# Optimization experiments

Hardware: AMD Instinct MI355X
Metric: run time of the kernel (lower is better)

Reference implementation:

```python
import jax, jax.numpy as jnp
import numpy as np


def setup_inputs() -> dict:
    key = jax.random.key(0)
    k1, k2, k3, k4 = jax.random.split(key, 4)
    b, c, h, w = 32, 512, 64, 64
    r = 16
    return {
        "x": jax.random.normal(k1, (b, c, h, w), dtype=jnp.float32),
        "mu": jax.random.uniform(k2, (b, 2), dtype=jnp.float32),
        "log_sigma_se": jnp.zeros((), dtype=jnp.float32),
        "w_fc1": jax.random.normal(k3, (c // r, c), dtype=jnp.float32) * 0.05,
        "w_fc2": jax.random.normal(k4, (c, c // r), dtype=jnp.float32) * 0.05,
    }


def reference(x, mu, log_sigma_se, w_fc1, w_fc2):
    b, c, h, w = x.shape
    sigma = jnp.exp(log_sigma_se)
    # grids in [0,1]; grid_x varies along h, grid_y along w ('ij' indexing)
    gx = jnp.linspace(0.0, 1.0, h)[:, None]          # (h,1)
    gy = jnp.linspace(0.0, 1.0, w)[None, :]          # (1,w)
    mu_h = mu[:, 0][:, None, None]                   # (b,1,1)
    mu_w = mu[:, 1][:, None, None]
    dx = gx[None, :, :] - mu_h                       # (b,h,w) via broadcast
    dy = gy[None, :, :] - mu_w
    kernel = jnp.exp(-(dx * dx + dy * dy) / (2.0 * sigma))   # (b,h,w)
    kernel = kernel / jnp.sum(kernel, axis=(1, 2), keepdims=True)
    squeezed = jnp.einsum('bchw,bhw->bc', x, kernel)          # (b,c)
    hid = jax.nn.relu(squeezed @ w_fc1.T)                     # (b,c//r)
    weights = jax.nn.sigmoid(hid @ w_fc2.T)                   # (b,c)
    return x * weights[:, :, None, None]
```

## Files before the change

### kernel.cpp

```cpp
#include <hip/hip_runtime.h>
#include <math.h>

#define BB 32
#define CC 512
#define HH 64
#define WW 64
#define RR 16
#define CR (CC / RR)
#define BPG 16
#define NGROUPS (BB / BPG)

typedef float floatx4 __attribute__((ext_vector_type(4)));

__device__ __forceinline__ float wave_sum64(float v) {
    #pragma unroll
    for (int off = 32; off > 0; off >>= 1)
        v += __shfl_xor(v, off, 64);
    return v;
}

__global__ void k_squeeze(const float* __restrict__ x,
                          const float* __restrict__ mu,
                          const float* __restrict__ log_sigma,
                          float* __restrict__ sq, int b0) {
    __shared__ float s_kx[64];
    __shared__ float s_ky[64];
    int b = b0 + blockIdx.y;
    int tid = threadIdx.x;

    if (tid < 64) {
        float sigma = expf(log_sigma[0]);
        float inv2s = 1.0f / (2.0f * sigma);
        float g = (float)tid / 63.0f;
        float dh = g - mu[b * 2 + 0];
        float dw = g - mu[b * 2 + 1];
        float vx = expf(-dh * dh * inv2s);
        float vy = expf(-dw * dw * inv2s);
        float sx = wave_sum64(vx);
        float sy = wave_sum64(vy);
        s_kx[tid] = vx / sx;
        s_ky[tid] = vy / sy;
    }
    __syncthreads();

    int wv = tid >> 6;
    int lane = tid & 63;
    int c = blockIdx.x * 4 + wv;
    const floatx4* xp = (const floatx4*)(x + ((size_t)(b * CC + c)) * (HH * WW));
    int col = lane & 15;
    int hbase = lane >> 4;
    float a0 = 0.f, a1 = 0.f, a2 = 0.f, a3 = 0.f;
    #pragma unroll
    for (int it = 0; it < 16; ++it) {
        int h = hbase + it * 4;
        floatx4 v = xp[h * 16 + col];
        float kh = s_kx[h];
        a0 += v.x * kh; a1 += v.y * kh; a2 += v.z * kh; a3 += v.w * kh;
    }
    int w0 = col * 4;
    float partial = a0 * s_ky[w0] + a1 * s_ky[w0 + 1] + a2 * s_ky[w0 + 2] + a3 * s_ky[w0 + 3];
    float s = wave_sum64(partial);
    if (lane == 0) sq[b * CC + c] = s;
}

__global__ void k_scale_fused(const float* __restrict__ x,
                              const float* __restrict__ sq,
                              const float* __restrict__ w1,
                              const float* __restrict__ w2,
                              float* __restrict__ out, int b0) {
    __shared__ float s_sq[CC];
    __shared__ float s_hid[CR];
    __shared__ float s_w[8];
    int b = b0 + blockIdx.y;
    int c0 = blockIdx.x * 8;
    int tid = threadIdx.x;

    for (int i = tid; i < CC; i += 256) s_sq[i] = sq[b * CC + i];
    __syncthreads();

    {
        int j = tid >> 3;
        int seg = tid & 7;
        float acc = 0.f;
        const float* w1r = w1 + j * CC + seg * 64;
        const float* sqr = s_sq + seg * 64;
        #pragma unroll 8
        for (int c = 0; c < 64; ++c) acc += sqr[c] * w1r[c];
        acc += __shfl_xor(acc, 4, 64);
        acc += __shfl_xor(acc, 2, 64);
        acc += __shfl_xor(acc, 1, 64);
        if (seg == 0) s_hid[j] = fmaxf(acc, 0.0f);
    }
    __syncthreads();

    if (tid < 8) {
        const float* w2r = w2 + (c0 + tid) * CR;
        float a = 0.f;
        #pragma unroll
        for (int jj = 0; jj < CR; ++jj) a += s_hid[jj] * w2r[jj];
        s_w[tid] = 1.0f / (1.0f + expf(-a));
    }
    __syncthreads();

    const floatx4* xp = (const floatx4*)(x + ((size_t)(b * CC + c0)) * (HH * WW));
    floatx4* op = (floatx4*)(out + ((size_t)(b * CC + c0)) * (HH * WW));
    #pragma unroll 8
    for (int it = 0; it < 32; ++it) {
        int idx = it * 256 + tid;
        float s = s_w[idx >> 10];
        floatx4 v = xp[idx];
        __builtin_nontemporal_store(v * s, op + idx);
    }
}

extern "C" void kernel_launch(void* const* d_in, const int* in_sizes, int n_in,
                              void* d_out, int out_size, void* d_ws, size_t ws_size,
                              hipStream_t stream) {
    const float* x  = (const float*)d_in[0];
    const float* mu = (const float*)d_in[1];
    const float* ls = (const float*)d_in[2];
    const float* w1 = (const float*)d_in[3];
    const float* w2 = (const float*)d_in[4];
    float* out = (float*)d_out;

    float* sq = (float*)d_ws;

    for (int g = 0; g < NGROUPS; ++g) {
        int b0 = g * BPG;
        k_squeeze<<<dim3(CC / 4, BPG), 256, 0, stream>>>(x, mu, ls, sq, b0);
        k_scale_fused<<<dim3(64, BPG), 256, 0, stream>>>(x, sq, w1, w2, out, b0);
    }
}
```

Measured before the change: 145.8 us.

## Fuse squeeze and scale into one cooperative kernel caching x in registers

Replaces the two per-group kernels with a single cooperative kernel. Each thread loads its slice of x once, keeps it in a 64-element vector register array, and computes the squeeze partial sums. A grid-wide sync follows, then the FC layers run and the cached values are scaled and written out. The aim is to drop the second read of x. The cost is heavy register pressure under __launch_bounds__(1024,4): the whole tensor exceeds the total register file, so spilling to scratch is likely, and a grid sync is added.

```diff
diff --git a/kernel.cpp b/kernel.cpp
--- a/kernel.cpp
+++ b/kernel.cpp
@@ -1,14 +1,14 @@
 #include <hip/hip_runtime.h>
+#include <hip/hip_cooperative_groups.h>
 #include <math.h>
+
+namespace cg = cooperative_groups;
 
 #define BB 32
 #define CC 512
 #define HH 64
 #define WW 64
-#define RR 16
-#define CR (CC / RR)
-#define BPG 16
-#define NGROUPS (BB / BPG)
+#define CR 32
 
 typedef float floatx4 __attribute__((ext_vector_type(4)));
 
@@ -19,19 +19,31 @@
     return v;
 }
 
-__global__ void k_squeeze(const float* __restrict__ x,
-                          const float* __restrict__ mu,
-                          const float* __restrict__ log_sigma,
-                          float* __restrict__ sq, int b0) {
+__global__ void __launch_bounds__(1024, 4)
+k_fused(const float* __restrict__ x,
+        const float* __restrict__ mu,
+        const float* __restrict__ log_sigma,
+        const float* __restrict__ w1,
+        const float* __restrict__ w2,
+        float* __restrict__ out,
+        float* __restrict__ sq_ws) {
     __shared__ float s_kx[64];
     __shared__ float s_ky[64];
-    int b = b0 + blockIdx.y;
-    int tid = threadIdx.x;
+    __shared__ float s_sq[CC];
+    __shared__ float s_hid[CR];
+    __shared__ float s_w[64];
+
+    const int bk  = blockIdx.x;
+    const int b   = bk >> 3;
+    const int cb  = (bk & 7) * 64;
+    const int tid = threadIdx.x;
+    const int w   = tid >> 6;
+    const int l   = tid & 63;
 
     if (tid < 64) {
         float sigma = expf(log_sigma[0]);
         float inv2s = 1.0f / (2.0f * sigma);
-        float g = (float)tid / 63.0f;
+        float g  = (float)tid / 63.0f;
         float dh = g - mu[b * 2 + 0];
         float dw = g - mu[b * 2 + 1];
         float vx = expf(-dh * dh * inv2s);
@@ -43,58 +55,52 @@
     }
     __syncthreads();
 
-    int wv = tid >> 6;
-    int lane = tid & 63;
-    int c = blockIdx.x * 4 + wv;
-    const floatx4* xp = (const floatx4*)(x + ((size_t)(b * CC + c)) * (HH * WW));
-    int col = lane & 15;
-    int hbase = lane >> 4;
-    float a0 = 0.f, a1 = 0.f, a2 = 0.f, a3 = 0.f;
+    const int col4 = l & 15;
+    const float ky0 = s_ky[col4 * 4 + 0];
+    const float ky1 = s_ky[col4 * 4 + 1];
+    const float ky2 = s_ky[col4 * 4 + 2];
+    const float ky3 = s_ky[col4 * 4 + 3];
+    float kxr[16];
     #pragma unroll
-    for (int it = 0; it < 16; ++it) {
-        int h = hbase + it * 4;
-        floatx4 v = xp[h * 16 + col];
-        float kh = s_kx[h];
-        a0 += v.x * kh; a1 += v.y * kh; a2 += v.z * kh; a3 += v.w * kh;
+    for (int m = 0; m < 16; ++m) kxr[m] = s_kx[m * 4 + (l >> 4)];
+
+    const size_t base = ((size_t)(b * CC + cb)) * 1024 + (size_t)w * 4096 + l;
+    const floatx4* xp = (const floatx4*)x;
+    floatx4 data[64];
+    float acc[4] = {0.f, 0.f, 0.f, 0.f};
+    #pragma unroll
+    for (int it = 0; it < 64; ++it) {
+        floatx4 v = xp[base + it * 64];
+        data[it] = v;
+        acc[it >> 4] += (v.x * ky0 + v.y * ky1 + v.z * ky2 + v.w * ky3) * kxr[it & 15];
     }
-    int w0 = col * 4;
-    float partial = a0 * s_ky[w0] + a1 * s_ky[w0 + 1] + a2 * s_ky[w0 + 2] + a3 * s_ky[w0 + 3];
-    float s = wave_sum64(partial);
-    if (lane == 0) sq[b * CC + c] = s;
-}
+    #pragma unroll
+    for (int k = 0; k < 4; ++k) {
+        float s = wave_sum64(acc[k]);
+        if (l == 0) sq_ws[b * CC + cb + w * 4 + k] = s;
+    }
 
-__global__ void k_scale_fused(const float* __restrict__ x,
-                              const float* __restrict__ sq,
-                              const float* __restrict__ w1,
-                              const float* __restrict__ w2,
-                              float* __restrict__ out, int b0) {
-    __shared__ float s_sq[CC];
-    __shared__ float s_hid[CR];
-    __shared__ float s_w[8];
-    int b = b0 + blockIdx.y;
-    int c0 = blockIdx.x * 8;
-    int tid = threadIdx.x;
+    __threadfence();
+    cg::this_grid().sync();
 
-    for (int i = tid; i < CC; i += 256) s_sq[i] = sq[b * CC + i];
+    if (tid < CC) s_sq[tid] = sq_ws[b * CC + tid];
     __syncthreads();
-
-    {
+    if (tid < 256) {
         int j = tid >> 3;
         int seg = tid & 7;
-        float acc = 0.f;
+        float a = 0.f;
         const float* w1r = w1 + j * CC + seg * 64;
         const float* sqr = s_sq + seg * 64;
         #pragma unroll 8
-        for (int c = 0; c < 64; ++c) acc += sqr[c] * w1r[c];
-        acc += __shfl_xor(acc, 4, 64);
-        acc += __shfl_xor(acc, 2, 64);
-        acc += __shfl_xor(acc, 1, 64);
-        if (seg == 0) s_hid[j] = fmaxf(acc, 0.0f);
+        for (int c = 0; c < 64; ++c) a += sqr[c] * w1r[c];
+        a += __shfl_xor(a, 4, 64);
+        a += __shfl_xor(a, 2, 64);
+        a += __shfl_xor(a, 1, 64);
+        if (seg == 0) s_hid[j] = fmaxf(a, 0.0f);
     }
     __syncthreads();
-
-    if (tid < 8) {
-        const float* w2r = w2 + (c0 + tid) * CR;
+    if (tid < 64) {
+        const float* w2r = w2 + (size_t)(cb + tid) * CR;
         float a = 0.f;
         #pragma unroll
         for (int jj = 0; jj < CR; ++jj) a += s_hid[jj] * w2r[jj];
@@ -102,14 +108,13 @@
     }
     __syncthreads();
 
-    const floatx4* xp = (const floatx4*)(x + ((size_t)(b * CC + c0)) * (HH * WW));
-    floatx4* op = (floatx4*)(out + ((size_t)(b * CC + c0)) * (HH * WW));
-    #pragma unroll 8
-    for (int it = 0; it < 32; ++it) {
-        int idx = it * 256 + tid;
-        float s = s_w[idx >> 10];
-        floatx4 v = xp[idx];
-        __builtin_nontemporal_store(v * s, op + idx);
+    float sc[4];
+    #pragma unroll
+    for (int k = 0; k < 4; ++k) sc[k] = s_w[w * 4 + k];
+    floatx4* op = (floatx4*)out;
+    #pragma unroll
+    for (int it = 0; it < 64; ++it) {
+        __builtin_nontemporal_store(data[it] * sc[it >> 4], op + base + it * 64);
     }
 }
 
@@ -122,12 +127,10 @@
     const float* w1 = (const float*)d_in[3];
     const float* w2 = (const float*)d_in[4];
     float* out = (float*)d_out;
+    float* sq  = (float*)d_ws;
 
-    float* sq = (float*)d_ws;
-
-    for (int g = 0; g < NGROUPS; ++g) {
-        int b0 = g * BPG;
-        k_squeeze<<<dim3(CC / 4, BPG), 256, 0, stream>>>(x, mu, ls, sq, b0);
-        k_scale_fused<<<dim3(64, BPG), 256, 0, stream>>>(x, sq, w1, w2, out, b0);
-    }
+    void* args[] = {(void*)&x, (void*)&mu, (void*)&ls, (void*)&w1,
+                    (void*)&w2, (void*)&out, (void*)&sq};
+    hipLaunchCooperativeKernel((const void*)k_fused, dim3(256), dim3(1024),
+                               args, 0, stream);
 }
```

Result: slower. 333.0 us (+128.5%).

## Cache fp16 copy of x during squeeze and scale from it

Applied to the files above, without the earlier changes.

The squeeze kernel also writes a half-precision copy of x into workspace, and the scale kernel reads that copy instead of the fp32 input, with a fallback when the workspace is too small. The per-batch-group launch split is removed so each kernel covers all batches. The intent is to cut read bandwidth in the second pass, but it adds a 128MB write, loses the L2/LLC reuse the batch grouping gave, and lowers the output precision to fp16.

```diff
diff --git a/kernel.cpp b/kernel.cpp
--- a/kernel.cpp
+++ b/kernel.cpp
@@ -3,14 +3,10 @@
 
 #define BB 32
 #define CC 512
-#define HH 64
-#define WW 64
-#define RR 16
-#define CR (CC / RR)
-#define BPG 16
-#define NGROUPS (BB / BPG)
+#define CR 32
 
-typedef float floatx4 __attribute__((ext_vector_type(4)));
+typedef float    floatx4 __attribute__((ext_vector_type(4)));
+typedef _Float16 halfx4  __attribute__((ext_vector_type(4)));
 
 __device__ __forceinline__ float wave_sum64(float v) {
     #pragma unroll
@@ -19,13 +15,15 @@
     return v;
 }
 
+template <bool WRITE_H>
 __global__ void k_squeeze(const float* __restrict__ x,
                           const float* __restrict__ mu,
                           const float* __restrict__ log_sigma,
-                          float* __restrict__ sq, int b0) {
+                          float* __restrict__ sq,
+                          _Float16* __restrict__ xh) {
     __shared__ float s_kx[64];
     __shared__ float s_ky[64];
-    int b = b0 + blockIdx.y;
+    int b = blockIdx.y;
     int tid = threadIdx.x;
 
     if (tid < 64) {
@@ -46,14 +44,22 @@
     int wv = tid >> 6;
     int lane = tid & 63;
     int c = blockIdx.x * 4 + wv;
-    const floatx4* xp = (const floatx4*)(x + ((size_t)(b * CC + c)) * (HH * WW));
+    const size_t chbase = ((size_t)(b * CC + c)) * 4096;
+    const floatx4* xp = (const floatx4*)(x + chbase);
+    halfx4* xhp = (halfx4*)(xh + chbase);
     int col = lane & 15;
     int hbase = lane >> 4;
     float a0 = 0.f, a1 = 0.f, a2 = 0.f, a3 = 0.f;
     #pragma unroll
     for (int it = 0; it < 16; ++it) {
         int h = hbase + it * 4;
-        floatx4 v = xp[h * 16 + col];
+        floatx4 v = __builtin_nontemporal_load(xp + h * 16 + col);
+        if (WRITE_H) {
+            halfx4 hh;
+            hh.x = (_Float16)v.x; hh.y = (_Float16)v.y;
+            hh.z = (_Float16)v.z; hh.w = (_Float16)v.w;
+            xhp[h * 16 + col] = hh;
+        }
         float kh = s_kx[h];
         a0 += v.x * kh; a1 += v.y * kh; a2 += v.z * kh; a3 += v.w * kh;
     }
@@ -63,47 +69,81 @@
     if (lane == 0) sq[b * CC + c] = s;
 }
 
-__global__ void k_scale_fused(const float* __restrict__ x,
-                              const float* __restrict__ sq,
-                              const float* __restrict__ w1,
-                              const float* __restrict__ w2,
-                              float* __restrict__ out, int b0) {
-    __shared__ float s_sq[CC];
-    __shared__ float s_hid[CR];
-    __shared__ float s_w[8];
-    int b = b0 + blockIdx.y;
-    int c0 = blockIdx.x * 8;
-    int tid = threadIdx.x;
-
+__device__ __forceinline__ void mlp_weights(const float* __restrict__ sq,
+                                            const float* __restrict__ w1,
+                                            const float* __restrict__ w2,
+                                            int b, int c0, int tid,
+                                            float* s_sq, float* s_hid, float* s_w) {
     for (int i = tid; i < CC; i += 256) s_sq[i] = sq[b * CC + i];
     __syncthreads();
-
     {
         int j = tid >> 3;
         int seg = tid & 7;
-        float acc = 0.f;
+        float a = 0.f;
         const float* w1r = w1 + j * CC + seg * 64;
         const float* sqr = s_sq + seg * 64;
         #pragma unroll 8
-        for (int c = 0; c < 64; ++c) acc += sqr[c] * w1r[c];
-        acc += __shfl_xor(acc, 4, 64);
-        acc += __shfl_xor(acc, 2, 64);
-        acc += __shfl_xor(acc, 1, 64);
-        if (seg == 0) s_hid[j] = fmaxf(acc, 0.0f);
+        for (int c = 0; c < 64; ++c) a += sqr[c] * w1r[c];
+        a += __shfl_xor(a, 4, 64);
+        a += __shfl_xor(a, 2, 64);
+        a += __shfl_xor(a, 1, 64);
+        if (seg == 0) s_hid[j] = fmaxf(a, 0.0f);
     }
     __syncthreads();
-
     if (tid < 8) {
-        const float* w2r = w2 + (c0 + tid) * CR;
+        const float* w2r = w2 + (size_t)(c0 + tid) * CR;
         float a = 0.f;
         #pragma unroll
         for (int jj = 0; jj < CR; ++jj) a += s_hid[jj] * w2r[jj];
         s_w[tid] = 1.0f / (1.0f + expf(-a));
     }
     __syncthreads();
+}
 
-    const floatx4* xp = (const floatx4*)(x + ((size_t)(b * CC + c0)) * (HH * WW));
-    floatx4* op = (floatx4*)(out + ((size_t)(b * CC + c0)) * (HH * WW));
+__global__ void k_scale_h(const _Float16* __restrict__ xh,
+                          const float* __restrict__ sq,
+                          const float* __restrict__ w1,
+                          const float* __restrict__ w2,
+                          float* __restrict__ out) {
+    __shared__ float s_sq[CC];
+    __shared__ float s_hid[CR];
+    __shared__ float s_w[8];
+    int b = blockIdx.y;
+    int c0 = blockIdx.x * 8;
+    int tid = threadIdx.x;
+    mlp_weights(sq, w1, w2, b, c0, tid, s_sq, s_hid, s_w);
+
+    const size_t base = ((size_t)(b * CC + c0)) * 4096;
+    const halfx4* xp = (const halfx4*)(xh + base);
+    floatx4* op = (floatx4*)(out + base);
+    #pragma unroll 8
+    for (int it = 0; it < 32; ++it) {
+        int idx = it * 256 + tid;
+        float s = s_w[idx >> 10];
+        halfx4 h = xp[idx];
+        floatx4 o;
+        o.x = (float)h.x * s; o.y = (float)h.y * s;
+        o.z = (float)h.z * s; o.w = (float)h.w * s;
+        __builtin_nontemporal_store(o, op + idx);
+    }
+}
+
+__global__ void k_scale_f(const float* __restrict__ x,
+                          const float* __restrict__ sq,
+                          const float* __restrict__ w1,
+                          const float* __restrict__ w2,
+                          float* __restrict__ out) {
+    __shared__ float s_sq[CC];
+    __shared__ float s_hid[CR];
+    __shared__ float s_w[8];
+    int b = blockIdx.y;
+    int c0 = blockIdx.x * 8;
+    int tid = threadIdx.x;
+    mlp_weights(sq, w1, w2, b, c0, tid, s_sq, s_hid, s_w);
+
+    const size_t base = ((size_t)(b * CC + c0)) * 4096;
+    const floatx4* xp = (const floatx4*)(x + base);
+    floatx4* op = (floatx4*)(out + base);
     #pragma unroll 8
     for (int it = 0; it < 32; ++it) {
         int idx = it * 256 + tid;
@@ -124,10 +164,14 @@
     float* out = (float*)d_out;
 
     float* sq = (float*)d_ws;
+    _Float16* xh = (_Float16*)((char*)d_ws + 65536);
+    size_t needed = 65536 + (size_t)BB * CC * 4096 * sizeof(_Float16);
 
-    for (int g = 0; g < NGROUPS; ++g) {
-        int b0 = g * BPG;
-        k_squeeze<<<dim3(CC / 4, BPG), 256, 0, stream>>>(x, mu, ls, sq, b0);
-        k_scale_fused<<<dim3(64, BPG), 256, 0, stream>>>(x, sq, w1, w2, out, b0);
+    if (ws_size >= needed) {
+        k_squeeze<true><<<dim3(CC / 4, BB), 256, 0, stream>>>(x, mu, ls, sq, xh);
+        k_scale_h<<<dim3(64, BB), 256, 0, stream>>>(xh, sq, w1, w2, out);
+    } else {
+        k_squeeze<false><<<dim3(CC / 4, BB), 256, 0, stream>>>(x, mu, ls, sq, nullptr);
+        k_scale_f<<<dim3(64, BB), 256, 0, stream>>>(x, sq, w1, w2, out);
     }
 }
```

Result: faster. 137.0 us (-6.0%).
